# Kernel tuning notes

Measured on AMD Instinct MI355X. Metric: run time of the kernel, lower is better.

The kernel has to match this reference:

```python
import jax, jax.numpy as jnp
import numpy as np
import math

B, C, N, L = 32, 128, 2048, 1
H, DK, APT = 8, 16, 10
EPS = 1e-5


def conv1x1(x, W, b):
    # 1x1 Conv2d on [B, C, N, L]
    return jnp.einsum('oc,bcnl->bonl', W, x) + b[None, :, None, None]


def layer_norm_12(x):
    # normalize over dims (1, 2) as in the custom LayerNorm (no affine)
    mean = x.mean(axis=(1, 2), keepdims=True)
    var = x.var(axis=(1, 2), keepdims=True)
    return (x - mean) / jnp.sqrt(var + EPS)


def setup_inputs() -> dict:
    key = jax.random.key(0)
    ks = jax.random.split(key, 10)
    s = 0.05  # small-scale init for numerical stability
    inp = {
        'input': jax.random.normal(ks[0], (B, C, N, L), jnp.float32),
        'Wq': jax.random.normal(ks[1], (C, C), jnp.float32) * s,
        'bq': jnp.zeros((C,), jnp.float32),
        'Wv': jax.random.normal(ks[2], (C, C), jnp.float32) * s,
        'bv': jnp.zeros((C,), jnp.float32),
        'Wc': jax.random.normal(ks[3], (C, C), jnp.float32) * s,
        'bc': jnp.zeros((C,), jnp.float32),
        'memory': jax.random.normal(ks[4], (H, L, N, DK), jnp.float32) * s,
        'sa_weight': jnp.ones((C, N, L), jnp.float32),
        'sa_bias': jnp.zeros((C, N, L), jnp.float32),
        'nodevec1': jax.random.normal(ks[5], (N, APT), jnp.float32),
        'nodevec2': jax.random.normal(ks[6], (APT, N), jnp.float32),
        'Wg1': jax.random.normal(ks[7], (C, C), jnp.float32) * s,
        'bg1': jnp.zeros((C,), jnp.float32),
        'Wg2': jax.random.normal(ks[8], (C, C), jnp.float32) * s,
        'bg2': jnp.zeros((C,), jnp.float32),
        'Wg3': jax.random.normal(ks[9], (C, C), jnp.float32) * s,
        'bg3': jnp.zeros((C,), jnp.float32),
    }
    return inp


def reference(input, Wq, bq, Wv, bv, Wc, bc, memory, sa_weight, sa_bias,
              nodevec1, nodevec2, Wg1, bg1, Wg2, bg2, Wg3, bg3):
    scale = math.sqrt(DK)

    def split_heads(t):  # [B,C,N,L] -> [B,H,L,N,DK]
        return t.reshape(B, H, DK, N, L).transpose(0, 1, 4, 3, 2)

    # SpatialAttention (Conv = 1x1 conv + relu; dropout off in eval)
    q = jax.nn.relu(conv1x1(input, Wq, bq))
    v = jax.nn.relu(conv1x1(input, Wv, bv))
    query = jax.nn.softmax(split_heads(q) / scale, axis=-1)     # [B,H,L,N,DK]
    value = split_heads(v)                                       # [B,H,L,N,DK]
    key = jax.nn.softmax(memory / scale, axis=-1)                # [H,L,N,DK]
    Aapt = jax.nn.softmax(jax.nn.relu(nodevec1 @ nodevec2), axis=-1)  # [N,N]

    kv = jnp.einsum('hlnx,bhlny->bhlxy', key, value)             # [B,H,L,DK,DK]
    attn_qkv = jnp.einsum('bhlnx,bhlxy->bhlny', query, kv)       # [B,H,L,N,DK]
    attn_dyn = jnp.einsum('nm,bhlnc->bhlnc', Aapt, value)        # row-sum scaling
    x = attn_qkv + attn_dyn

    # merge heads back to [B,C,N,L] and apply concat conv (Conv = conv+relu)
    x = x.transpose(0, 1, 4, 3, 2).reshape(B, C, N, L)
    x = jax.nn.relu(conv1x1(x, Wc, bc))
    x = x * sa_weight[None] + sa_bias[None] + x                  # affine branch

    # Encoder wrap
    x = x + input
    x = layer_norm_12(x)
    g = conv1x1(x, Wg1, bg1) * jax.nn.sigmoid(conv1x1(x, Wg2, bg2))
    g = conv1x1(g, Wg3, bg3)                                     # GLU
    x = g + x
    x = x * sa_weight[None] + sa_bias[None] + x
    x = layer_norm_12(x)
    return x
```

## Files before the change

kernel.cpp:

```cpp
#include <hip/hip_runtime.h>
#include <hip/hip_bf16.h>
#include <math.h>

#define DI __device__ __forceinline__

typedef short bf16x8 __attribute__((ext_vector_type(8)));
typedef float f32x4 __attribute__((ext_vector_type(4)));

constexpr int BB = 32, CC = 128, NN = 2048;
constexpr float EPSf = 1e-5f;
constexpr float RCN = 1.0f / (CC * (float)NN);

#define MFMA(a,b,c) __builtin_amdgcn_mfma_f32_16x16x32_bf16(a,b,c,0,0,0)

DI unsigned short f2b(float f){
    union { __hip_bfloat16 h; unsigned short u; } v;
    v.h = __float2bfloat16(f);
    return v.u;
}
DI float b2f(unsigned short h){
    union { unsigned u; float f; } v; v.u = ((unsigned)h) << 16;
    return v.f;
}
DI float sigm(float x){ return 1.0f / (1.0f + __expf(-x)); }

__global__ __launch_bounds__(256) void k_prep(
    const float* __restrict__ Wq, const float* __restrict__ Wv,
    const float* __restrict__ Wc, const float* __restrict__ Wg1,
    const float* __restrict__ Wg2, const float* __restrict__ Wg3,
    unsigned short* __restrict__ Wb, float* __restrict__ rs)
{
    const int tid = threadIdx.x;
    if (blockIdx.x < 96) {
        const int i = blockIdx.x * 256 + tid;
        const int m = i >> 12, q = i & 4095;
        const float* src = (m==0)?Wq:(m==1)?Wv:(m==2)?Wc:(m==3)?Wg1:(m==4)?Wg2:Wg3;
        f32x4 w = *(const f32x4*)&src[q * 4];
        ushort4 p; p.x=f2b(w[0]); p.y=f2b(w[1]); p.z=f2b(w[2]); p.w=f2b(w[3]);
        *(ushort4*)&Wb[(size_t)m * 16384 + q * 4] = p;
    } else {
        const float* src = (tid < 128) ? Wg1 : Wg2;
        const int o = tid & 127;
        float s = 0.f;
#pragma unroll
        for (int j = 0; j < 32; j++) {
            f32x4 a = *(const f32x4*)&src[o * 128 + j * 4];
            s += a[0] + a[1] + a[2] + a[3];
        }
        rs[tid] = s;
    }
}

__global__ __launch_bounds__(256) void k_keysm(const float* __restrict__ mem,
                                               unsigned short* __restrict__ ksT)
{
    const int row = blockIdx.x * 256 + threadIdx.x;
    const int h = row >> 11, n = row & 2047;
    const float* p = mem + (size_t)row * 16;
    float v[16];
    f32x4 t0 = *(const f32x4*)(p);
    f32x4 t1 = *(const f32x4*)(p + 4);
    f32x4 t2 = *(const f32x4*)(p + 8);
    f32x4 t3 = *(const f32x4*)(p + 12);
#pragma unroll
    for (int j = 0; j < 4; j++) { v[j]=t0[j]; v[4+j]=t1[j]; v[8+j]=t2[j]; v[12+j]=t3[j]; }
    float mx = v[0];
#pragma unroll
    for (int x = 1; x < 16; x++) mx = fmaxf(mx, v[x]);
    float s = 0.f;
#pragma unroll
    for (int x = 0; x < 16; x++) { v[x] = __expf((v[x] - mx) * 0.25f); s += v[x]; }
    const float is = 1.0f / s;
#pragma unroll
    for (int x = 0; x < 16; x++)
        ksT[((size_t)(h * 16 + x)) * NN + n] = f2b(v[x] * is);
}

__global__ __launch_bounds__(256,2) void k_qv(
    const float* __restrict__ in, const unsigned short* __restrict__ WqB,
    const unsigned short* __restrict__ WvB, const float* __restrict__ bq,
    const float* __restrict__ bv, unsigned short* __restrict__ qT,
    unsigned short* __restrict__ vT)
{
    const int b = blockIdx.x >> 4, n0 = (blockIdx.x & 15) * 128;
    const int tid = threadIdx.x, l = tid & 63, wid = tid >> 6;
    const int wo = wid & 1, wn = wid >> 1, lr = l & 15, lg = l >> 4;
    f32x4 accq[4][4], accv[4][4];
    const f32x4 z = {0.f,0.f,0.f,0.f};
#pragma unroll
    for (int i = 0; i < 4; i++)
#pragma unroll
        for (int j = 0; j < 4; j++) { accq[i][j] = z; accv[i][j] = z; }
    const float* inb = in + (size_t)b * CC * NN;
#pragma unroll
    for (int ks = 0; ks < 4; ks++) {
        const int cb = ks * 32 + lg * 8;
        bf16x8 aq[4], av[4];
#pragma unroll
        for (int mf = 0; mf < 4; mf++) {
            const int o = wo*64 + mf*16 + lr;
            aq[mf] = *(const bf16x8*)&WqB[o * 128 + cb];
            av[mf] = *(const bf16x8*)&WvB[o * 128 + cb];
        }
        bf16x8 bx[4];
#pragma unroll
        for (int nf = 0; nf < 4; nf++) {
            const int n = n0 + wn*64 + nf*16 + lr;
            union { bf16x8 v; unsigned short u[8]; } t;
#pragma unroll
            for (int j = 0; j < 8; j++) t.u[j] = f2b(inb[(size_t)(cb + j) * NN + n]);
            bx[nf] = t.v;
        }
#pragma unroll
        for (int mf = 0; mf < 4; mf++)
#pragma unroll
            for (int nf = 0; nf < 4; nf++) {
                accq[mf][nf] = MFMA(aq[mf], bx[nf], accq[mf][nf]);
                accv[mf][nf] = MFMA(av[mf], bx[nf], accv[mf][nf]);
            }
    }
#pragma unroll
    for (int mf = 0; mf < 4; mf++) {
        const int ob = wo*64 + mf*16 + lg*4;
        const f32x4 bq4 = *(const f32x4*)&bq[ob];
        const f32x4 bv4 = *(const f32x4*)&bv[ob];
#pragma unroll
        for (int nf = 0; nf < 4; nf++) {
            const int n = n0 + wn*64 + nf*16 + lr;
            const size_t yo = ((size_t)b * NN + n) * CC + ob;
            f32x4 aq_ = accq[mf][nf], av_ = accv[mf][nf];
            ushort4 pq, pv;
            pq.x = f2b(fmaxf(aq_[0]+bq4[0],0.f)); pq.y = f2b(fmaxf(aq_[1]+bq4[1],0.f));
            pq.z = f2b(fmaxf(aq_[2]+bq4[2],0.f)); pq.w = f2b(fmaxf(aq_[3]+bq4[3],0.f));
            pv.x = f2b(fmaxf(av_[0]+bv4[0],0.f)); pv.y = f2b(fmaxf(av_[1]+bv4[1],0.f));
            pv.z = f2b(fmaxf(av_[2]+bv4[2],0.f)); pv.w = f2b(fmaxf(av_[3]+bv4[3],0.f));
            *(ushort4*)&qT[yo] = pq;
            *(ushort4*)&vT[yo] = pv;
        }
    }
}

__global__ __launch_bounds__(256) void k_kv(const unsigned short* __restrict__ ksT,
                                            const unsigned short* __restrict__ vT,
                                            float* __restrict__ kvb)
{
    __shared__ unsigned short vt[4 * 16 * 520];
    __shared__ float red[1024];
    const int b = blockIdx.x >> 3, h = blockIdx.x & 7;
    const int tid = threadIdx.x, l = tid & 63, wid = tid >> 6;
    const int n0 = wid * 512;
    unsigned short* vtw = vt + wid * (16 * 520);
    const unsigned short* vb = vT + ((size_t)b * NN + n0) * CC + h * 16;
#pragma unroll
    for (int r = 0; r < 8; r++) {
        const int nl = r * 64 + l;
        ushort4 p0 = *(const ushort4*)&vb[(size_t)nl * CC + 0];
        ushort4 p1 = *(const ushort4*)&vb[(size_t)nl * CC + 4];
        ushort4 p2 = *(const ushort4*)&vb[(size_t)nl * CC + 8];
        ushort4 p3 = *(const ushort4*)&vb[(size_t)nl * CC + 12];
        vtw[ 0*520+nl]=p0.x; vtw[ 1*520+nl]=p0.y; vtw[ 2*520+nl]=p0.z; vtw[ 3*520+nl]=p0.w;
        vtw[ 4*520+nl]=p1.x; vtw[ 5*520+nl]=p1.y; vtw[ 6*520+nl]=p1.z; vtw[ 7*520+nl]=p1.w;
        vtw[ 8*520+nl]=p2.x; vtw[ 9*520+nl]=p2.y; vtw[10*520+nl]=p2.z; vtw[11*520+nl]=p2.w;
        vtw[12*520+nl]=p3.x; vtw[13*520+nl]=p3.y; vtw[14*520+nl]=p3.z; vtw[15*520+nl]=p3.w;
    }
    const int lr = l & 15, lg = l >> 4;
    const unsigned short* ka = ksT + (size_t)h * 16 * NN;
    f32x4 acc = {0.f,0.f,0.f,0.f};
#pragma unroll
    for (int kk = 0; kk < 16; kk++) {
        bf16x8 af = *(const bf16x8*)&ka[(size_t)lr * NN + n0 + kk*32 + lg*8];
        bf16x8 bf = *(const bf16x8*)&vtw[lr * 520 + kk*32 + lg*8];
        acc = MFMA(af, bf, acc);
    }
#pragma unroll
    for (int r = 0; r < 4; r++)
        red[wid * 256 + (lg*4 + r) * 16 + lr] = acc[r];
    __syncthreads();
    {
        const float s = red[tid] + red[256 + tid] + red[512 + tid] + red[768 + tid];
        kvb[((size_t)(b * 8 + h)) * 256 + tid] = s;
    }
}

__global__ __launch_bounds__(256,2) void k_attnC(
    const unsigned short* __restrict__ qT, unsigned short* __restrict__ vT,
    const float* __restrict__ kvb, const unsigned short* __restrict__ WcB,
    const float* __restrict__ bc, const float* __restrict__ saw,
    const float* __restrict__ sab, const float* __restrict__ in0f,
    float* __restrict__ part1)
{
    __shared__ float kvl[8 * 260];
    __shared__ unsigned short xc[128 * 136];
    __shared__ float red[8];
    const int b = blockIdx.x >> 4, n0 = (blockIdx.x & 15) * 128;
    const int tid = threadIdx.x;
    {
        const float* kp = kvb + (size_t)b * 2048 + (tid >> 5) * 256 + (tid & 31) * 8;
        f32x4 v0 = *(const f32x4*)kp;
        f32x4 v1 = *(const f32x4*)(kp + 4);
        float* dst = &kvl[(tid >> 5) * 260 + (tid & 31) * 8];
        *(f32x4*)dst = v0; *(f32x4*)(dst + 4) = v1;
    }
    __syncthreads();
#pragma unroll
    for (int it = 0; it < 4; it++) {
        const int idx = it * 256 + tid;
        const int nl = idx >> 3, h = idx & 7;
        const size_t base = ((size_t)b * NN + n0 + nl) * CC + h * 16;
        const unsigned short* qp = qT + base;
        const unsigned short* vp = vT + base;
        float q[16];
        {
            uint4 u0 = *(const uint4*)qp, u1 = *(const uint4*)(qp + 8);
            unsigned uu[8] = {u0.x,u0.y,u0.z,u0.w,u1.x,u1.y,u1.z,u1.w};
#pragma unroll
            for (int j = 0; j < 8; j++) {
                q[2*j]   = b2f((unsigned short)(uu[j] & 0xffffu));
                q[2*j+1] = b2f((unsigned short)(uu[j] >> 16));
            }
        }
        float mx = q[0];
#pragma unroll
        for (int x = 1; x < 16; x++) mx = fmaxf(mx, q[x]);
        float p[16]; float s = 0.f;
#pragma unroll
        for (int x = 0; x < 16; x++) { p[x] = __expf((q[x] - mx) * 0.25f); s += p[x]; }
        const float is = 1.0f / s;
        const float* kh = &kvl[h * 260];
        float r[16];
#pragma unroll
        for (int y = 0; y < 16; y++) r[y] = 0.f;
#pragma unroll
        for (int x = 0; x < 16; x++) {
            const float px = p[x];
#pragma unroll
            for (int y = 0; y < 16; y++) r[y] = fmaf(px, kh[x * 16 + y], r[y]);
        }
        uint4 w0 = *(const uint4*)vp, w1 = *(const uint4*)(vp + 8);
        unsigned vv[8] = {w0.x,w0.y,w0.z,w0.w,w1.x,w1.y,w1.z,w1.w};
        unsigned short* xp = &xc[nl * 136 + h * 16];
#pragma unroll
        for (int j2 = 0; j2 < 4; j2++) {
            ushort4 pk;
            pk.x = f2b(r[4*j2+0]*is + b2f((unsigned short)(vv[2*j2]   & 0xffffu)));
            pk.y = f2b(r[4*j2+1]*is + b2f((unsigned short)(vv[2*j2]   >> 16)));
            pk.z = f2b(r[4*j2+2]*is + b2f((unsigned short)(vv[2*j2+1] & 0xffffu)));
            pk.w = f2b(r[4*j2+3]*is + b2f((unsigned short)(vv[2*j2+1] >> 16)));
            *(ushort4*)&xp[j2 * 4] = pk;
        }
    }
    __syncthreads();
    const int l = tid & 63, wid = tid >> 6;
    const int wo = wid & 1, wn = wid >> 1, lr = l & 15, lg = l >> 4;
    f32x4 acc[4][4];
    const f32x4 z = {0.f,0.f,0.f,0.f};
#pragma unroll
    for (int i = 0; i < 4; i++)
#pragma unroll
        for (int j = 0; j < 4; j++) acc[i][j] = z;
#pragma unroll
    for (int ks = 0; ks < 4; ks++) {
        const int cb = ks * 32 + lg * 8;
        bf16x8 af[4];
#pragma unroll
        for (int mf = 0; mf < 4; mf++)
            af[mf] = *(const bf16x8*)&WcB[(wo*64 + mf*16 + lr) * 128 + cb];
        bf16x8 bx[4];
#pragma unroll
        for (int nf = 0; nf < 4; nf++)
            bx[nf] = *(const bf16x8*)&xc[(wn*64 + nf*16 + lr) * 136 + cb];
#pragma unroll
        for (int mf = 0; mf < 4; mf++)
#pragma unroll
            for (int nf = 0; nf < 4; nf++)
                acc[mf][nf] = MFMA(af[mf], bx[nf], acc[mf][nf]);
    }
    float sum = 0.f, ssq = 0.f;
#pragma unroll
    for (int mf = 0; mf < 4; mf++) {
        const int ob = wo*64 + mf*16 + lg*4;
        const f32x4 b4 = *(const f32x4*)&bc[ob];
#pragma unroll
        for (int nf = 0; nf < 4; nf++) {
            const int n = n0 + wn*64 + nf*16 + lr;
            const size_t yo = ((size_t)b * NN + n) * CC + ob;
            f32x4 a = acc[mf][nf];
            float ys[4];
#pragma unroll
            for (int r = 0; r < 4; r++) {
                const int o = ob + r;
                const float t = fmaxf(a[r] + b4[r], 0.f);
                const float sw = saw[(size_t)o * NN + n];
                const float sb = sab[(size_t)o * NN + n];
                float y = t * sw + sb + t + in0f[((size_t)b * CC + o) * NN + n];
                sum += y; ssq += y * y;
                ys[r] = y;
            }
            ushort4 pk;
            pk.x = f2b(ys[0]); pk.y = f2b(ys[1]); pk.z = f2b(ys[2]); pk.w = f2b(ys[3]);
            *(ushort4*)&vT[yo] = pk;
        }
    }
#pragma unroll
    for (int off = 32; off > 0; off >>= 1) {
        sum += __shfl_down(sum, off);
        ssq += __shfl_down(ssq, off);
    }
    if ((tid & 63) == 0) { red[wid*2] = sum; red[wid*2+1] = ssq; }
    __syncthreads();
    if (tid == 0) {
        part1[2 * blockIdx.x]     = red[0]+red[2]+red[4]+red[6];
        part1[2 * blockIdx.x + 1] = red[1]+red[3]+red[5]+red[7];
    }
}

__global__ __launch_bounds__(256,2) void k_glu3(
    const unsigned short* __restrict__ y1,
    const unsigned short* __restrict__ W1B, const unsigned short* __restrict__ W2B,
    const unsigned short* __restrict__ W3B,
    const float* __restrict__ b1, const float* __restrict__ b2,
    const float* __restrict__ b3, const float* __restrict__ rs,
    const float* __restrict__ part1, const float* __restrict__ saw,
    const float* __restrict__ sab, unsigned short* __restrict__ X2,
    float* __restrict__ part2)
{
    __shared__ unsigned short yt[128 * 136];
    __shared__ unsigned short gx[128 * 136];
    __shared__ float cs[256];
    __shared__ float red[8];
    const int b = blockIdx.x >> 4, n0 = (blockIdx.x & 15) * 128;
    const int tid = threadIdx.x;
    float s0 = 0.f, q0 = 0.f;
#pragma unroll
    for (int t = 0; t < 16; t++) { s0 += part1[(b*16+t)*2]; q0 += part1[(b*16+t)*2+1]; }
    const float mean = s0 * RCN;
    const float var  = q0 * RCN - mean * mean;
    const float inv  = rsqrtf(var + EPSf);
    {
        const int cq = tid & 15;
#pragma unroll
        for (int it = 0; it < 8; it++) {
            const int n = it * 16 + (tid >> 4);
            uint4 u = *(const uint4*)&y1[((size_t)b * NN + n0 + n) * CC + cq * 8];
            *(uint4*)&yt[n * 136 + cq * 8] = u;
        }
    }
    {
        const int o = tid & 127;
        const float bb = (tid < 128) ? b1[o] : b2[o];
        cs[tid] = bb - mean * inv * rs[tid];
    }
    __syncthreads();
    const int l = tid & 63, wid = tid >> 6;
    const int wo = wid & 1, wn = wid >> 1, lr = l & 15, lg = l >> 4;
    {
        f32x4 acc1[4][4], acc2[4][4];
        const f32x4 z = {0.f,0.f,0.f,0.f};
#pragma unroll
        for (int i = 0; i < 4; i++)
#pragma unroll
            for (int j = 0; j < 4; j++) { acc1[i][j] = z; acc2[i][j] = z; }
#pragma unroll
        for (int ks = 0; ks < 4; ks++) {
            const int cb = ks * 32 + lg * 8;
            bf16x8 a1[4], a2[4];
#pragma unroll
            for (int mf = 0; mf < 4; mf++) {
                const int o = wo*64 + mf*16 + lr;
                a1[mf] = *(const bf16x8*)&W1B[o * 128 + cb];
                a2[mf] = *(const bf16x8*)&W2B[o * 128 + cb];
            }
            bf16x8 bx[4];
#pragma unroll
            for (int nf = 0; nf < 4; nf++)
                bx[nf] = *(const bf16x8*)&yt[(wn*64 + nf*16 + lr) * 136 + cb];
#pragma unroll
            for (int mf = 0; mf < 4; mf++)
#pragma unroll
                for (int nf = 0; nf < 4; nf++) {
                    acc1[mf][nf] = MFMA(a1[mf], bx[nf], acc1[mf][nf]);
                    acc2[mf][nf] = MFMA(a2[mf], bx[nf], acc2[mf][nf]);
                }
        }
#pragma unroll
        for (int mf = 0; mf < 4; mf++) {
            const int ob = wo*64 + mf*16 + lg*4;
            const f32x4 c1 = *(const f32x4*)&cs[ob];
            const f32x4 c2 = *(const f32x4*)&cs[128 + ob];
#pragma unroll
            for (int nf = 0; nf < 4; nf++) {
                const int nl = wn*64 + nf*16 + lr;
                ushort4 pk;
                float g1, g2;
                g1 = acc1[mf][nf][0]*inv + c1[0]; g2 = acc2[mf][nf][0]*inv + c2[0];
                pk.x = f2b(g1 * sigm(g2));
                g1 = acc1[mf][nf][1]*inv + c1[1]; g2 = acc2[mf][nf][1]*inv + c2[1];
                pk.y = f2b(g1 * sigm(g2));
                g1 = acc1[mf][nf][2]*inv + c1[2]; g2 = acc2[mf][nf][2]*inv + c2[2];
                pk.z = f2b(g1 * sigm(g2));
                g1 = acc1[mf][nf][3]*inv + c1[3]; g2 = acc2[mf][nf][3]*inv + c2[3];
                pk.w = f2b(g1 * sigm(g2));
                *(ushort4*)&gx[nl * 136 + ob] = pk;
            }
        }
    }
    __syncthreads();
    f32x4 acc[4][4];
    const f32x4 z = {0.f,0.f,0.f,0.f};
#pragma unroll
    for (int i = 0; i < 4; i++)
#pragma unroll
        for (int j = 0; j < 4; j++) acc[i][j] = z;
#pragma unroll
    for (int ks = 0; ks < 4; ks++) {
        const int cb = ks * 32 + lg * 8;
        bf16x8 af[4];
#pragma unroll
        for (int mf = 0; mf < 4; mf++)
            af[mf] = *(const bf16x8*)&W3B[(wo*64 + mf*16 + lr) * 128 + cb];
        bf16x8 bx[4];
#pragma unroll
        for (int nf = 0; nf < 4; nf++)
            bx[nf] = *(const bf16x8*)&gx[(wn*64 + nf*16 + lr) * 136 + cb];
#pragma unroll
        for (int mf = 0; mf < 4; mf++)
#pragma unroll
            for (int nf = 0; nf < 4; nf++)
                acc[mf][nf] = MFMA(af[mf], bx[nf], acc[mf][nf]);
    }
    float sum = 0.f, ssq = 0.f;
#pragma unroll
    for (int mf = 0; mf < 4; mf++) {
        const int ob = wo*64 + mf*16 + lg*4;
        const f32x4 b4 = *(const f32x4*)&b3[ob];
#pragma unroll
        for (int nf = 0; nf < 4; nf++) {
            const int nl = wn*64 + nf*16 + lr;
            const int n = n0 + nl;
            const size_t yo = ((size_t)b * NN + n) * CC + ob;
            ushort4 yq = *(const ushort4*)&yt[nl * 136 + ob];
            f32x4 a = acc[mf][nf];
            float ys[4];
#pragma unroll
            for (int r = 0; r < 4; r++) {
                const int o = ob + r;
                const unsigned short ev = (r==0)?yq.x:(r==1)?yq.y:(r==2)?yq.z:yq.w;
                const float t = a[r] + b4[r] + (b2f(ev) - mean) * inv;
                const float sw = saw[(size_t)o * NN + n];
                const float sb = sab[(size_t)o * NN + n];
                const float y = t * sw + sb + t;
                sum += y; ssq += y * y;
                ys[r] = y;
            }
            ushort4 pk;
            pk.x = f2b(ys[0]); pk.y = f2b(ys[1]); pk.z = f2b(ys[2]); pk.w = f2b(ys[3]);
            *(ushort4*)&X2[yo] = pk;
        }
    }
#pragma unroll
    for (int off = 32; off > 0; off >>= 1) {
        sum += __shfl_down(sum, off);
        ssq += __shfl_down(ssq, off);
    }
    if ((tid & 63) == 0) { red[wid*2] = sum; red[wid*2+1] = ssq; }
    __syncthreads();
    if (tid == 0) {
        part2[2 * blockIdx.x]     = red[0]+red[2]+red[4]+red[6];
        part2[2 * blockIdx.x + 1] = red[1]+red[3]+red[5]+red[7];
    }
}

__global__ __launch_bounds__(256) void k_lnfin(const unsigned short* __restrict__ x2,
                                               const float* __restrict__ part2,
                                               float* __restrict__ out)
{
    __shared__ unsigned ts[64 * 69];
    const int b = blockIdx.x >> 5, n0 = (blockIdx.x & 31) * 64;
    const int tid = threadIdx.x;
    float s0 = 0.f, q0 = 0.f;
#pragma unroll
    for (int t = 0; t < 16; t++) { s0 += part2[(b*16+t)*2]; q0 += part2[(b*16+t)*2+1]; }
    const float mean = s0 * RCN;
    const float var  = q0 * RCN - mean * mean;
    const float inv  = rsqrtf(var + EPSf);
    {
        const int n = tid >> 2, qd = tid & 3;
        const unsigned short* src = x2 + ((size_t)b * NN + n0 + n) * CC + qd * 32;
        uint4 a0 = *(const uint4*)(src);
        uint4 a1 = *(const uint4*)(src + 8);
        uint4 a2 = *(const uint4*)(src + 16);
        uint4 a3 = *(const uint4*)(src + 24);
        unsigned u[16] = {a0.x,a0.y,a0.z,a0.w, a1.x,a1.y,a1.z,a1.w,
                          a2.x,a2.y,a2.z,a2.w, a3.x,a3.y,a3.z,a3.w};
#pragma unroll
        for (int k = 0; k < 16; k++)
            ts[(qd * 16 + k) * 69 + n] = u[k];
    }
    __syncthreads();
#pragma unroll
    for (int pass = 0; pass < 8; pass++) {
        const int c = pass * 16 + (tid >> 4), nq = tid & 15;
        const int cp = c >> 1, hi = c & 1;
        f32x4 v;
#pragma unroll
        for (int j = 0; j < 4; j++) {
            const unsigned u = ts[cp * 69 + nq * 4 + j];
            const unsigned short hv = hi ? (unsigned short)(u >> 16)
                                         : (unsigned short)(u & 0xffffu);
            v[j] = (b2f(hv) - mean) * inv;
        }
        *(f32x4*)&out[((size_t)b * CC + c) * NN + n0 + nq * 4] = v;
    }
}

extern "C" void kernel_launch(void* const* d_in, const int* in_sizes, int n_in,
                              void* d_out, int out_size, void* d_ws, size_t ws_size,
                              hipStream_t stream)
{
    const float* input = (const float*)d_in[0];
    const float* Wq  = (const float*)d_in[1];
    const float* bq  = (const float*)d_in[2];
    const float* Wv  = (const float*)d_in[3];
    const float* bv  = (const float*)d_in[4];
    const float* Wc  = (const float*)d_in[5];
    const float* bc  = (const float*)d_in[6];
    const float* mem = (const float*)d_in[7];
    const float* saw = (const float*)d_in[8];
    const float* sab = (const float*)d_in[9];
    const float* Wg1 = (const float*)d_in[12];
    const float* bg1 = (const float*)d_in[13];
    const float* Wg2 = (const float*)d_in[14];
    const float* bg2 = (const float*)d_in[15];
    const float* Wg3 = (const float*)d_in[16];
    const float* bg3 = (const float*)d_in[17];
    float* out = (float*)d_out;

    unsigned char* wsb = (unsigned char*)d_ws;
    unsigned short* qT  = (unsigned short*)(wsb);
    unsigned short* vT  = (unsigned short*)(wsb + 16777216);
    unsigned short* ksT = (unsigned short*)(wsb + 33554432);
    float* kvb   = (float*)(wsb + 34078720);
    unsigned short* Wb  = (unsigned short*)(wsb + 34340864);
    float* rs    = (float*)(wsb + 34537472);
    float* part1 = (float*)(wsb + 34538496);
    float* part2 = (float*)(wsb + 34542592);

    k_prep <<<97,   256, 0, stream>>>(Wq, Wv, Wc, Wg1, Wg2, Wg3, Wb, rs);
    k_keysm<<<64,   256, 0, stream>>>(mem, ksT);
    k_qv   <<<512,  256, 0, stream>>>(input, Wb, Wb + 16384, bq, bv, qT, vT);
    k_kv   <<<256,  256, 0, stream>>>(ksT, vT, kvb);
    k_attnC<<<512,  256, 0, stream>>>(qT, vT, kvb, Wb + 2*16384, bc, saw, sab,
                                      input, part1);
    k_glu3 <<<512,  256, 0, stream>>>(vT, Wb + 3*16384, Wb + 4*16384, Wb + 5*16384,
                                      bg1, bg2, bg3, rs, part1, saw, sab, qT, part2);
    k_lnfin<<<1024, 256, 0, stream>>>(qT, part2, out);
}
```

Measured before the change: 135.4 us.

## Stage epilogue outputs through LDS for coalesced stores; merge key softmax into prep

The epilogues of the q/v projection, attention-concat and GLU kernels now write their bf16 tiles into shared memory first and then store full 16-byte rows to global memory, replacing scattered 8-byte stores. The key-softmax kernel is folded into the weight-prep kernel, which removes one launch. The kv kernel reads V with 16-byte loads, and the attention kernel's launch bound occupancy hint goes from 2 to 3. The cost is extra barriers and LDS traffic, and the higher occupancy hint may add register pressure or spills.

Measured after the change: 184.6 us. +36.4%, slower.

```diff
diff --git a/kernel.cpp b/kernel.cpp
--- a/kernel.cpp
+++ b/kernel.cpp
@@ -28,7 +28,9 @@
     const float* __restrict__ Wq, const float* __restrict__ Wv,
     const float* __restrict__ Wc, const float* __restrict__ Wg1,
     const float* __restrict__ Wg2, const float* __restrict__ Wg3,
-    unsigned short* __restrict__ Wb, float* __restrict__ rs)
+    const float* __restrict__ mem,
+    unsigned short* __restrict__ Wb, float* __restrict__ rs,
+    unsigned short* __restrict__ ksT)
 {
     const int tid = threadIdx.x;
     if (blockIdx.x < 96) {
@@ -38,7 +40,7 @@
         f32x4 w = *(const f32x4*)&src[q * 4];
         ushort4 p; p.x=f2b(w[0]); p.y=f2b(w[1]); p.z=f2b(w[2]); p.w=f2b(w[3]);
         *(ushort4*)&Wb[(size_t)m * 16384 + q * 4] = p;
-    } else {
+    } else if (blockIdx.x == 96) {
         const float* src = (tid < 128) ? Wg1 : Wg2;
         const int o = tid & 127;
         float s = 0.f;
@@ -48,32 +50,28 @@
             s += a[0] + a[1] + a[2] + a[3];
         }
         rs[tid] = s;
-    }
-}
-
-__global__ __launch_bounds__(256) void k_keysm(const float* __restrict__ mem,
-                                               unsigned short* __restrict__ ksT)
-{
-    const int row = blockIdx.x * 256 + threadIdx.x;
-    const int h = row >> 11, n = row & 2047;
-    const float* p = mem + (size_t)row * 16;
-    float v[16];
-    f32x4 t0 = *(const f32x4*)(p);
-    f32x4 t1 = *(const f32x4*)(p + 4);
-    f32x4 t2 = *(const f32x4*)(p + 8);
-    f32x4 t3 = *(const f32x4*)(p + 12);
-#pragma unroll
-    for (int j = 0; j < 4; j++) { v[j]=t0[j]; v[4+j]=t1[j]; v[8+j]=t2[j]; v[12+j]=t3[j]; }
-    float mx = v[0];
-#pragma unroll
-    for (int x = 1; x < 16; x++) mx = fmaxf(mx, v[x]);
-    float s = 0.f;
-#pragma unroll
-    for (int x = 0; x < 16; x++) { v[x] = __expf((v[x] - mx) * 0.25f); s += v[x]; }
-    const float is = 1.0f / s;
-#pragma unroll
-    for (int x = 0; x < 16; x++)
-        ksT[((size_t)(h * 16 + x)) * NN + n] = f2b(v[x] * is);
+    } else {
+        const int row = (blockIdx.x - 97) * 256 + tid;
+        const int h = row >> 11, n = row & 2047;
+        const float* p = mem + (size_t)row * 16;
+        float v[16];
+        f32x4 t0 = *(const f32x4*)(p);
+        f32x4 t1 = *(const f32x4*)(p + 4);
+        f32x4 t2 = *(const f32x4*)(p + 8);
+        f32x4 t3 = *(const f32x4*)(p + 12);
+#pragma unroll
+        for (int j = 0; j < 4; j++) { v[j]=t0[j]; v[4+j]=t1[j]; v[8+j]=t2[j]; v[12+j]=t3[j]; }
+        float mx = v[0];
+#pragma unroll
+        for (int x = 1; x < 16; x++) mx = fmaxf(mx, v[x]);
+        float s = 0.f;
+#pragma unroll
+        for (int x = 0; x < 16; x++) { v[x] = __expf((v[x] - mx) * 0.25f); s += v[x]; }
+        const float is = 1.0f / s;
+#pragma unroll
+        for (int x = 0; x < 16; x++)
+            ksT[((size_t)(h * 16 + x)) * NN + n] = f2b(v[x] * is);
+    }
 }
 
 __global__ __launch_bounds__(256,2) void k_qv(
@@ -82,6 +80,7 @@
     const float* __restrict__ bv, unsigned short* __restrict__ qT,
     unsigned short* __restrict__ vT)
 {
+    __shared__ unsigned short tile[128 * 136];
     const int b = blockIdx.x >> 4, n0 = (blockIdx.x & 15) * 128;
     const int tid = threadIdx.x, l = tid & 63, wid = tid >> 6;
     const int wo = wid & 1, wn = wid >> 1, lr = l & 15, lg = l >> 4;
@@ -122,21 +121,45 @@
 #pragma unroll
     for (int mf = 0; mf < 4; mf++) {
         const int ob = wo*64 + mf*16 + lg*4;
-        const f32x4 bq4 = *(const f32x4*)&bq[ob];
-        const f32x4 bv4 = *(const f32x4*)&bv[ob];
+        const f32x4 b4 = *(const f32x4*)&bq[ob];
 #pragma unroll
         for (int nf = 0; nf < 4; nf++) {
-            const int n = n0 + wn*64 + nf*16 + lr;
-            const size_t yo = ((size_t)b * NN + n) * CC + ob;
-            f32x4 aq_ = accq[mf][nf], av_ = accv[mf][nf];
-            ushort4 pq, pv;
-            pq.x = f2b(fmaxf(aq_[0]+bq4[0],0.f)); pq.y = f2b(fmaxf(aq_[1]+bq4[1],0.f));
-            pq.z = f2b(fmaxf(aq_[2]+bq4[2],0.f)); pq.w = f2b(fmaxf(aq_[3]+bq4[3],0.f));
-            pv.x = f2b(fmaxf(av_[0]+bv4[0],0.f)); pv.y = f2b(fmaxf(av_[1]+bv4[1],0.f));
-            pv.z = f2b(fmaxf(av_[2]+bv4[2],0.f)); pv.w = f2b(fmaxf(av_[3]+bv4[3],0.f));
-            *(ushort4*)&qT[yo] = pq;
-            *(ushort4*)&vT[yo] = pv;
-        }
+            const int nl = wn*64 + nf*16 + lr;
+            f32x4 a = accq[mf][nf];
+            ushort4 pk;
+            pk.x = f2b(fmaxf(a[0]+b4[0],0.f)); pk.y = f2b(fmaxf(a[1]+b4[1],0.f));
+            pk.z = f2b(fmaxf(a[2]+b4[2],0.f)); pk.w = f2b(fmaxf(a[3]+b4[3],0.f));
+            *(ushort4*)&tile[nl * 136 + ob] = pk;
+        }
+    }
+    __syncthreads();
+#pragma unroll
+    for (int p = 0; p < 8; p++) {
+        const int row = p*16 + (tid >> 4), col = (tid & 15) * 8;
+        *(uint4*)&qT[((size_t)b * NN + n0 + row) * CC + col] =
+            *(const uint4*)&tile[row * 136 + col];
+    }
+    __syncthreads();
+#pragma unroll
+    for (int mf = 0; mf < 4; mf++) {
+        const int ob = wo*64 + mf*16 + lg*4;
+        const f32x4 b4 = *(const f32x4*)&bv[ob];
+#pragma unroll
+        for (int nf = 0; nf < 4; nf++) {
+            const int nl = wn*64 + nf*16 + lr;
+            f32x4 a = accv[mf][nf];
+            ushort4 pk;
+            pk.x = f2b(fmaxf(a[0]+b4[0],0.f)); pk.y = f2b(fmaxf(a[1]+b4[1],0.f));
+            pk.z = f2b(fmaxf(a[2]+b4[2],0.f)); pk.w = f2b(fmaxf(a[3]+b4[3],0.f));
+            *(ushort4*)&tile[nl * 136 + ob] = pk;
+        }
+    }
+    __syncthreads();
+#pragma unroll
+    for (int p = 0; p < 8; p++) {
+        const int row = p*16 + (tid >> 4), col = (tid & 15) * 8;
+        *(uint4*)&vT[((size_t)b * NN + n0 + row) * CC + col] =
+            *(const uint4*)&tile[row * 136 + col];
     }
 }
 
@@ -154,14 +177,14 @@
 #pragma unroll
     for (int r = 0; r < 8; r++) {
         const int nl = r * 64 + l;
-        ushort4 p0 = *(const ushort4*)&vb[(size_t)nl * CC + 0];
-        ushort4 p1 = *(const ushort4*)&vb[(size_t)nl * CC + 4];
-        ushort4 p2 = *(const ushort4*)&vb[(size_t)nl * CC + 8];
-        ushort4 p3 = *(const ushort4*)&vb[(size_t)nl * CC + 12];
-        vtw[ 0*520+nl]=p0.x; vtw[ 1*520+nl]=p0.y; vtw[ 2*520+nl]=p0.z; vtw[ 3*520+nl]=p0.w;
-        vtw[ 4*520+nl]=p1.x; vtw[ 5*520+nl]=p1.y; vtw[ 6*520+nl]=p1.z; vtw[ 7*520+nl]=p1.w;
-        vtw[ 8*520+nl]=p2.x; vtw[ 9*520+nl]=p2.y; vtw[10*520+nl]=p2.z; vtw[11*520+nl]=p2.w;
-        vtw[12*520+nl]=p3.x; vtw[13*520+nl]=p3.y; vtw[14*520+nl]=p3.z; vtw[15*520+nl]=p3.w;
+        uint4 q0 = *(const uint4*)&vb[(size_t)nl * CC];
+        uint4 q1 = *(const uint4*)&vb[(size_t)nl * CC + 8];
+        const unsigned uu[8] = {q0.x,q0.y,q0.z,q0.w,q1.x,q1.y,q1.z,q1.w};
+#pragma unroll
+        for (int k = 0; k < 8; k++) {
+            vtw[(2*k)*520 + nl]   = (unsigned short)(uu[k] & 0xffffu);
+            vtw[(2*k+1)*520 + nl] = (unsigned short)(uu[k] >> 16);
+        }
     }
     const int lr = l & 15, lg = l >> 4;
     const unsigned short* ka = ksT + (size_t)h * 16 * NN;
@@ -182,7 +205,7 @@
     }
 }
 
-__global__ __launch_bounds__(256,2) void k_attnC(
+__global__ __launch_bounds__(256,3) void k_attnC(
     const unsigned short* __restrict__ qT, unsigned short* __restrict__ vT,
     const float* __restrict__ kvb, const unsigned short* __restrict__ WcB,
     const float* __restrict__ bc, const float* __restrict__ saw,
@@ -275,6 +298,7 @@
             for (int nf = 0; nf < 4; nf++)
                 acc[mf][nf] = MFMA(af[mf], bx[nf], acc[mf][nf]);
     }
+    __syncthreads();
     float sum = 0.f, ssq = 0.f;
 #pragma unroll
     for (int mf = 0; mf < 4; mf++) {
@@ -282,8 +306,8 @@
         const f32x4 b4 = *(const f32x4*)&bc[ob];
 #pragma unroll
         for (int nf = 0; nf < 4; nf++) {
-            const int n = n0 + wn*64 + nf*16 + lr;
-            const size_t yo = ((size_t)b * NN + n) * CC + ob;
+            const int nl = wn*64 + nf*16 + lr;
+            const int n = n0 + nl;
             f32x4 a = acc[mf][nf];
             float ys[4];
 #pragma unroll
@@ -298,8 +322,15 @@
             }
             ushort4 pk;
             pk.x = f2b(ys[0]); pk.y = f2b(ys[1]); pk.z = f2b(ys[2]); pk.w = f2b(ys[3]);
-            *(ushort4*)&vT[yo] = pk;
-        }
+            *(ushort4*)&xc[nl * 136 + ob] = pk;
+        }
+    }
+    __syncthreads();
+#pragma unroll
+    for (int p = 0; p < 8; p++) {
+        const int row = p*16 + (tid >> 4), col = (tid & 15) * 8;
+        *(uint4*)&vT[((size_t)b * NN + n0 + row) * CC + col] =
+            *(const uint4*)&xc[row * 136 + col];
     }
 #pragma unroll
     for (int off = 32; off > 0; off >>= 1) {
@@ -428,6 +459,7 @@
             for (int nf = 0; nf < 4; nf++)
                 acc[mf][nf] = MFMA(af[mf], bx[nf], acc[mf][nf]);
     }
+    __syncthreads();
     float sum = 0.f, ssq = 0.f;
 #pragma unroll
     for (int mf = 0; mf < 4; mf++) {
@@ -437,7 +469,6 @@
         for (int nf = 0; nf < 4; nf++) {
             const int nl = wn*64 + nf*16 + lr;
             const int n = n0 + nl;
-            const size_t yo = ((size_t)b * NN + n) * CC + ob;
             ushort4 yq = *(const ushort4*)&yt[nl * 136 + ob];
             f32x4 a = acc[mf][nf];
             float ys[4];
@@ -454,8 +485,15 @@
             }
             ushort4 pk;
             pk.x = f2b(ys[0]); pk.y = f2b(ys[1]); pk.z = f2b(ys[2]); pk.w = f2b(ys[3]);
-            *(ushort4*)&X2[yo] = pk;
-        }
+            *(ushort4*)&gx[nl * 136 + ob] = pk;
+        }
+    }
+    __syncthreads();
+#pragma unroll
+    for (int p = 0; p < 8; p++) {
+        const int row = p*16 + (tid >> 4), col = (tid & 15) * 8;
+        *(uint4*)&X2[((size_t)b * NN + n0 + row) * CC + col] =
+            *(const uint4*)&gx[row * 136 + col];
     }
 #pragma unroll
     for (int off = 32; off > 0; off >>= 1) {
@@ -545,8 +583,7 @@
     float* part1 = (float*)(wsb + 34538496);
     float* part2 = (float*)(wsb + 34542592);
 
-    k_prep <<<97,   256, 0, stream>>>(Wq, Wv, Wc, Wg1, Wg2, Wg3, Wb, rs);
-    k_keysm<<<64,   256, 0, stream>>>(mem, ksT);
+    k_prep <<<161,  256, 0, stream>>>(Wq, Wv, Wc, Wg1, Wg2, Wg3, mem, Wb, rs, ksT);
     k_qv   <<<512,  256, 0, stream>>>(input, Wb, Wb + 16384, bq, bv, qT, vT);
     k_kv   <<<256,  256, 0, stream>>>(ksT, vT, kvb);
     k_attnC<<<512,  256, 0, stream>>>(qT, vT, kvb, Wb + 2*16384, bc, saw, sab,
```
